# Kernel optimization log

Hardware: AMD Instinct MI355X
Metric: run time of the kernel (lower is better)

Reference implementation:

```python
import jax, jax.numpy as jnp
import numpy as np
import math

H, HD = 16, 64
EPS = 1e-6


def setup_inputs() -> dict:
    key = jax.random.key(0)
    ks = jax.random.split(key, 6)
    B, T, D = 4, 2048, 1024
    s = 0.02
    return {
        "x": jax.random.normal(ks[0], (B, T, D), jnp.float32),
        "wq": jax.random.normal(ks[1], (D, D), jnp.float32) * s,
        "wk": jax.random.normal(ks[2], (D, D), jnp.float32) * s,
        "wv": jax.random.normal(ks[3], (D, D), jnp.float32) * s,
        "wo": jax.random.normal(ks[4], (D, D), jnp.float32) * s,
        "norm_g": jnp.ones((D,), jnp.float32),
    }


def reference(x, wq, wk, wv, wo, norm_g):
    B, T, D = x.shape
    scale = math.sqrt(HD)
    # nn.Linear(D, D, bias=False): y = x @ W.T
    q = (x @ wq.T).reshape(B, T, H, HD).transpose(0, 2, 1, 3)  # [B,H,T,HD]
    k = (x @ wk.T).reshape(B, T, H, HD).transpose(0, 2, 1, 3)
    v = (x @ wv.T).reshape(B, T, H, HD).transpose(0, 2, 1, 3)
    scores = jnp.einsum("bhqd,bhkd->bhqk", q, k) / scale  # [B,H,T,T]
    causal = jnp.tril(jnp.ones((T, T), bool))  # True where allowed
    scores = jnp.where(causal, scores, -jnp.inf)
    attn = jax.nn.softmax(scores, axis=-1)  # dropout p=0 -> identity
    out = jnp.einsum("bhqk,bhkd->bhqd", attn, v)  # [B,H,T,HD]
    out = out.transpose(0, 2, 1, 3).reshape(B, T, D)
    y = x + out @ wo.T  # residual
    # RMSNorm
    rms = jnp.sqrt(jnp.mean(y * y, axis=-1, keepdims=True) + EPS)
    return (y / rms) * norm_g
```

## Files before the change

### kernel.cpp

```cpp
#include <hip/hip_runtime.h>
#include <hip/hip_bf16.h>

constexpr int NB  = 4;
constexpr int NT  = 2048;
constexpr int ND  = 1024;
constexpr int NH  = 16;
constexpr int NHD = 64;
constexpr int NM  = NB * NT;

typedef unsigned short u16;
typedef __attribute__((ext_vector_type(8))) short  short8;
typedef __attribute__((ext_vector_type(4))) float  f32x4;

__device__ __forceinline__ u16 f2bf(float f) {
  unsigned u = __builtin_bit_cast(unsigned, f);
  u += 0x7FFFu + ((u >> 16) & 1u);
  return (u16)(u >> 16);
}

__device__ __forceinline__ unsigned pk2bf(float lo, float hi_) {
  float2 t; t.x = lo; t.y = hi_;
  __hip_bfloat162 h2 = __float22bfloat162_rn(t);
  unsigned u;
  __builtin_memcpy(&u, &h2, 4);
  return u;
}

__device__ __forceinline__ void gll16(const u16* src, u16* dst) {
  __builtin_amdgcn_global_load_lds(
      (const __attribute__((address_space(1))) void*)src,
      (__attribute__((address_space(3))) void*)dst, 16, 0, 0);
}

__global__ __launch_bounds__(256) void cast_kernel(const float* __restrict__ in,
                                                   u16* __restrict__ out, int n4) {
  int i = blockIdx.x * 256 + threadIdx.x;
  if (i >= n4) return;
  float4 v = ((const float4*)in)[i];
  ushort4 o;
  o.x = f2bf(v.x); o.y = f2bf(v.y); o.z = f2bf(v.z); o.w = f2bf(v.w);
  ((ushort4*)out)[i] = o;
}

__global__ __launch_bounds__(256) void cast4_kernel(
    const float* __restrict__ w0, const float* __restrict__ w1,
    const float* __restrict__ w2, const float* __restrict__ w3,
    u16* __restrict__ o0, u16* __restrict__ o1,
    u16* __restrict__ o2, u16* __restrict__ o3) {
  const int z = blockIdx.x >> 10;
  const float* in = (z == 0) ? w0 : (z == 1) ? w1 : (z == 2) ? w2 : w3;
  u16* out       = (z == 0) ? o0 : (z == 1) ? o1 : (z == 2) ? o2 : o3;
  int i = (blockIdx.x & 1023) * 256 + threadIdx.x;
  float4 v = ((const float4*)in)[i];
  ushort4 o;
  o.x = f2bf(v.x); o.y = f2bf(v.y); o.z = f2bf(v.z); o.w = f2bf(v.w);
  ((ushort4*)out)[i] = o;
}

__global__ __launch_bounds__(512, 2) void gemm_qkv3(
    const u16* __restrict__ xb,
    const u16* __restrict__ wqb, const u16* __restrict__ wkb, const u16* __restrict__ wvb,
    u16* __restrict__ Qb, u16* __restrict__ Kb, u16* __restrict__ VTb) {
  const int z    = blockIdx.z;
  const int row0 = blockIdx.x << 7;
  const int col0 = blockIdx.y << 7;

  const u16* wsel = (z == 0) ? wqb : (z == 1) ? wkb : wvb;
  u16* osel      = (z == 0) ? Qb  : (z == 1) ? Kb  : VTb;
  const float scl = (z == 0) ? 0.125f * 1.44269504f : 1.0f;

  const int tid  = threadIdx.x;
  const int lane = tid & 63, wid = tid >> 6;
  const int wm = wid >> 2, wn = wid & 3;
  const int li = lane & 15, hi = lane >> 4;
  const int l3 = lane >> 3, sl = lane & 7;
  const int schunk = ((sl ^ l3) << 3);

  extern __shared__ __align__(16) u16 smem[];
  u16* lAb = smem;
  u16* lBb = smem + 3 * 128 * 64;

  auto stage = [&](int t) {
    const int bo = (t % 3) * 8192;
    const int k0 = t << 6;
#pragma unroll
    for (int h = 0; h < 2; ++h) {
      int r = h * 64 + wid * 8;
      gll16(&xb  [(size_t)(row0 + r + l3) * ND + k0 + schunk], &lAb[bo + r * 64]);
      gll16(&wsel[(size_t)(col0 + r + l3) * ND + k0 + schunk], &lBb[bo + r * 64]);
    }
  };

  f32x4 acc[4][2] = {};

  stage(0);
  stage(1);

  for (int i = 0; i < 16; ++i) {
    if (i < 15) { asm volatile("s_waitcnt vmcnt(4)" ::: "memory"); }
    else        { asm volatile("s_waitcnt vmcnt(0)" ::: "memory"); }
    __builtin_amdgcn_s_barrier();

    if (i + 2 < 16) stage(i + 2);

    const u16* la = &lAb[(i % 3) * 8192];
    const u16* lb = &lBb[(i % 3) * 8192];

    short8 a[4][2], b[2][2];
#pragma unroll
    for (int m = 0; m < 4; ++m)
#pragma unroll
      for (int c = 0; c < 2; ++c)
        a[m][c] = *(const short8*)&la[(wm * 64 + m * 16 + li) * 64 + (((c * 4 + hi) ^ (li & 7)) << 3)];
#pragma unroll
    for (int n = 0; n < 2; ++n)
#pragma unroll
      for (int c = 0; c < 2; ++c)
        b[n][c] = *(const short8*)&lb[(wn * 32 + n * 16 + li) * 64 + (((c * 4 + hi) ^ (li & 7)) << 3)];

    if (z == 2) {
#pragma unroll
      for (int m = 0; m < 4; ++m)
#pragma unroll
        for (int n = 0; n < 2; ++n)
#pragma unroll
          for (int c = 0; c < 2; ++c)
            acc[m][n] = __builtin_amdgcn_mfma_f32_16x16x32_bf16(a[m][c], b[n][c], acc[m][n], 0, 0, 0);
    } else {
#pragma unroll
      for (int m = 0; m < 4; ++m)
#pragma unroll
        for (int n = 0; n < 2; ++n)
#pragma unroll
          for (int c = 0; c < 2; ++c)
            acc[m][n] = __builtin_amdgcn_mfma_f32_16x16x32_bf16(b[n][c], a[m][c], acc[m][n], 0, 0, 0);
    }
  }

#pragma unroll
  for (int m = 0; m < 4; ++m)
#pragma unroll
    for (int n = 0; n < 2; ++n) {
      if (z == 2) {
        int token0 = row0 + wm * 64 + m * 16 + hi * 4;
        int col    = col0 + wn * 32 + n * 16 + li;
        int b_ = token0 >> 11, t0 = token0 & (NT - 1);
        int h_ = col >> 6,     d_ = col & (NHD - 1);
        uint2 w;
        w.x = pk2bf(acc[m][n][0], acc[m][n][1]);
        w.y = pk2bf(acc[m][n][2], acc[m][n][3]);
        *(uint2*)&osel[(((size_t)(b_ * NH + h_)) * NHD + d_) * NT + t0] = w;
      } else {
        int token = row0 + wm * 64 + m * 16 + li;
        int feat0 = col0 + wn * 32 + n * 16 + hi * 4;
        int b_ = token >> 11, t_ = token & (NT - 1);
        int h_ = feat0 >> 6,  d0 = feat0 & (NHD - 1);
        uint2 w;
        w.x = pk2bf(acc[m][n][0] * scl, acc[m][n][1] * scl);
        w.y = pk2bf(acc[m][n][2] * scl, acc[m][n][3] * scl);
        *(uint2*)&osel[(((size_t)(b_ * NH + h_)) * NT + t_) * NHD + d0] = w;
      }
    }
}

__global__ __launch_bounds__(512, 2) void gemm_wo3(
    const u16* __restrict__ ao, const u16* __restrict__ wob,
    const float* __restrict__ x, float* __restrict__ y) {
  const int row0 = blockIdx.x << 7;
  const int col0 = blockIdx.y << 7;

  const int tid  = threadIdx.x;
  const int lane = tid & 63, wid = tid >> 6;
  const int wm = wid >> 2, wn = wid & 3;
  const int li = lane & 15, hi = lane >> 4;
  const int l3 = lane >> 3, sl = lane & 7;
  const int schunk = ((sl ^ l3) << 3);

  extern __shared__ __align__(16) u16 smem[];
  u16* lAb = smem;
  u16* lBb = smem + 3 * 128 * 64;

  auto stage = [&](int t) {
    const int bo = (t % 3) * 8192;
    const int k0 = t << 6;
#pragma unroll
    for (int h = 0; h < 2; ++h) {
      int r = h * 64 + wid * 8;
      gll16(&ao [(size_t)(row0 + r + l3) * ND + k0 + schunk], &lAb[bo + r * 64]);
      gll16(&wob[(size_t)(col0 + r + l3) * ND + k0 + schunk], &lBb[bo + r * 64]);
    }
  };

  f32x4 acc[4][2] = {};

  stage(0);
  stage(1);

  for (int i = 0; i < 16; ++i) {
    if (i < 15) { asm volatile("s_waitcnt vmcnt(4)" ::: "memory"); }
    else        { asm volatile("s_waitcnt vmcnt(0)" ::: "memory"); }
    __builtin_amdgcn_s_barrier();

    if (i + 2 < 16) stage(i + 2);

    const u16* la = &lAb[(i % 3) * 8192];
    const u16* lb = &lBb[(i % 3) * 8192];

    short8 a[4][2], b[2][2];
#pragma unroll
    for (int m = 0; m < 4; ++m)
#pragma unroll
      for (int c = 0; c < 2; ++c)
        a[m][c] = *(const short8*)&la[(wm * 64 + m * 16 + li) * 64 + (((c * 4 + hi) ^ (li & 7)) << 3)];
#pragma unroll
    for (int n = 0; n < 2; ++n)
#pragma unroll
      for (int c = 0; c < 2; ++c)
        b[n][c] = *(const short8*)&lb[(wn * 32 + n * 16 + li) * 64 + (((c * 4 + hi) ^ (li & 7)) << 3)];

#pragma unroll
    for (int m = 0; m < 4; ++m)
#pragma unroll
      for (int n = 0; n < 2; ++n)
#pragma unroll
        for (int c = 0; c < 2; ++c)
          acc[m][n] = __builtin_amdgcn_mfma_f32_16x16x32_bf16(b[n][c], a[m][c], acc[m][n], 0, 0, 0);
  }

#pragma unroll
  for (int m = 0; m < 4; ++m)
#pragma unroll
    for (int n = 0; n < 2; ++n) {
      int token = row0 + wm * 64 + m * 16 + li;
      int feat0 = col0 + wn * 32 + n * 16 + hi * 4;
      size_t idx = (size_t)token * ND + feat0;
      float4 xv = *(const float4*)&x[idx];
      float4 o;
      o.x = acc[m][n][0] + xv.x; o.y = acc[m][n][1] + xv.y;
      o.z = acc[m][n][2] + xv.z; o.w = acc[m][n][3] + xv.w;
      *(float4*)&y[idx] = o;
    }
}

__global__ __launch_bounds__(256) void attn_kernel(
    const u16* __restrict__ Q, const u16* __restrict__ K, const u16* __restrict__ VT,
    u16* __restrict__ AO) {
  const int nb  = gridDim.x * gridDim.y;
  const int b0  = blockIdx.y * gridDim.x + blockIdx.x;
  const int L   = (b0 & 7) * (nb >> 3) + (b0 >> 3);
  const int qb  = 31 - (L & 31);
  const int bh  = L >> 5;

  const int tid = threadIdx.x;
  const int lane = tid & 63, wid = tid >> 6;
  const int li = lane & 15, hi = lane >> 4;
  const int r0 = qb * 64 + wid * 16;
  const int qrow = r0 + li;
  const size_t bK = (size_t)bh * NT * NHD;
  const size_t bV = (size_t)bh * NHD * NT;

  __shared__ __align__(16) u16 lK [2][64 * 64];
  __shared__ __align__(16) u16 lVT[2][64 * 64];
  __shared__ __align__(16) u16 lP [4][16 * 64];

  const int ch0 = tid, ch1 = tid + 256;
  const int d0 = (ch0 >> 3) * 64 + (((ch0 & 7) ^ ((ch0 >> 3) & 7)) << 3);
  const int d1 = (ch1 >> 3) * 64 + (((ch1 & 7) ^ ((ch1 >> 3) & 7)) << 3);
  const int vOff0 = (ch0 >> 3) * NT + (ch0 & 7) * 8;
  const int vOff1 = (ch1 >> 3) * NT + (ch1 & 7) * 8;

  uint4 gK0, gK1, gV0, gV1;
  auto issue = [&](int kt) {
    const u16* kp = K + bK + (size_t)kt * 4096;
    const u16* vp = VT + bV + kt * 64;
    gK0 = *(const uint4*)&kp[ch0 * 8];
    gK1 = *(const uint4*)&kp[ch1 * 8];
    gV0 = *(const uint4*)&vp[vOff0];
    gV1 = *(const uint4*)&vp[vOff1];
  };
  auto commit = [&](int buf) {
    *(uint4*)&lK [buf][d0] = gK0;
    *(uint4*)&lK [buf][d1] = gK1;
    *(uint4*)&lVT[buf][d0] = gV0;
    *(uint4*)&lVT[buf][d1] = gV1;
  };

  short8 qf[2];
#pragma unroll
  for (int c = 0; c < 2; ++c)
    qf[c] = *(const short8*)&Q[bK + (size_t)qrow * NHD + c * 32 + hi * 8];

  short8 vone;
#pragma unroll
  for (int e = 0; e < 8; ++e) vone[e] = (short)0x3F80;

  f32x4 o[4] = {};
  f32x4 o4 = {};

  issue(0);
  commit(0);
  __syncthreads();
  int buf = 0;

  const int pswz = (li & 7) << 1;

  for (int kt = 0; kt <= qb; ++kt) {
    if (kt < qb) issue(kt + 1);

    f32x4 s[4] = {};
    __builtin_amdgcn_s_setprio(1);
#pragma unroll
    for (int g = 0; g < 4; ++g)
#pragma unroll
      for (int c = 0; c < 2; ++c) {
        short8 kf = *(const short8*)&lK[buf][(g * 16 + li) * 64 + ((c * 4 + hi) ^ (li & 7)) * 8];
        s[g] = __builtin_amdgcn_mfma_f32_16x16x32_bf16(kf, qf[c], s[g], 0, 0, 0);
      }
    __builtin_amdgcn_s_setprio(0);

    if (kt == qb) {
#pragma unroll
      for (int g = 0; g < 4; ++g)
#pragma unroll
        for (int rg = 0; rg < 4; ++rg) {
          int kcol = kt * 64 + g * 16 + hi * 4 + rg;
          if (kcol > qrow) s[g][rg] = -INFINITY;
        }
    }

#pragma unroll
    for (int g = 0; g < 4; ++g) {
      float p0 = __builtin_amdgcn_exp2f(s[g][0]);
      float p1 = __builtin_amdgcn_exp2f(s[g][1]);
      float p2 = __builtin_amdgcn_exp2f(s[g][2]);
      float p3 = __builtin_amdgcn_exp2f(s[g][3]);
      uint2 w;
      w.x = pk2bf(p0, p1);
      w.y = pk2bf(p2, p3);
      int k8s = (g * 4 + hi) ^ pswz;
      *(uint2*)&lP[wid][li * 64 + k8s * 4] = w;
    }

    short8 pa[2];
#pragma unroll
    for (int c = 0; c < 2; ++c)
      pa[c] = *(const short8*)&lP[wid][li * 64 + ((c * 8 + hi * 2) ^ pswz) * 4];

    __builtin_amdgcn_s_setprio(1);
#pragma unroll
    for (int gd = 0; gd < 4; ++gd)
#pragma unroll
      for (int c = 0; c < 2; ++c) {
        short8 vf = *(const short8*)&lVT[buf][(gd * 16 + li) * 64 + ((c * 4 + hi) ^ (li & 7)) * 8];
        o[gd] = __builtin_amdgcn_mfma_f32_16x16x32_bf16(vf, pa[c], o[gd], 0, 0, 0);
      }
#pragma unroll
    for (int c = 0; c < 2; ++c)
      o4 = __builtin_amdgcn_mfma_f32_16x16x32_bf16(vone, pa[c], o4, 0, 0, 0);
    __builtin_amdgcn_s_setprio(0);

    if (kt < qb) commit(buf ^ 1);
    __syncthreads();
    buf ^= 1;
  }

  const int b_ = bh >> 4, h_ = bh & 15;
  const float inv = 1.0f / o4[0];
  const size_t rowbase = ((size_t)(b_ * NT + qrow)) * ND + h_ * 64;
#pragma unroll
  for (int gd = 0; gd < 4; ++gd) {
    uint2 w;
    w.x = pk2bf(o[gd][0] * inv, o[gd][1] * inv);
    w.y = pk2bf(o[gd][2] * inv, o[gd][3] * inv);
    *(uint2*)&AO[rowbase + gd * 16 + hi * 4] = w;
  }
}

__global__ __launch_bounds__(256) void rmsnorm_kernel(float* __restrict__ y,
                                                      const float* __restrict__ g) {
  const int row = blockIdx.x;
  const int tid = threadIdx.x;
  const int lane = tid & 63, wid = tid >> 6;
  float4 v = ((const float4*)(y + (size_t)row * ND))[tid];
  float ss = v.x * v.x + v.y * v.y + v.z * v.z + v.w * v.w;
#pragma unroll
  for (int off = 32; off; off >>= 1) ss += __shfl_down(ss, off);
  __shared__ float red[4];
  if (lane == 0) red[wid] = ss;
  __syncthreads();
  float tot = red[0] + red[1] + red[2] + red[3];
  float inv = rsqrtf(tot * (1.0f / (float)ND) + 1e-6f);
  float4 gg = ((const float4*)g)[tid];
  float4 o;
  o.x = v.x * inv * gg.x; o.y = v.y * inv * gg.y;
  o.z = v.z * inv * gg.z; o.w = v.w * inv * gg.w;
  ((float4*)(y + (size_t)row * ND))[tid] = o;
}

extern "C" void kernel_launch(void* const* d_in, const int* in_sizes, int n_in,
                              void* d_out, int out_size, void* d_ws, size_t ws_size,
                              hipStream_t stream) {
  const float* x  = (const float*)d_in[0];
  const float* wq = (const float*)d_in[1];
  const float* wk = (const float*)d_in[2];
  const float* wv = (const float*)d_in[3];
  const float* wo = (const float*)d_in[4];
  const float* ng = (const float*)d_in[5];
  float* out = (float*)d_out;

  char* ws = (char*)d_ws;
  u16* xb  = (u16*)(ws);
  u16* wqb = (u16*)(ws + (16u << 20));
  u16* wkb = (u16*)(ws + (18u << 20));
  u16* wvb = (u16*)(ws + (20u << 20));
  u16* wob = (u16*)(ws + (22u << 20));
  u16* Qb  = (u16*)(ws + (24u << 20));
  u16* Kb  = (u16*)(ws + (40u << 20));
  u16* VTb = (u16*)(ws + (56u << 20));
  u16* AO  = (u16*)(ws + (72u << 20));

  cast_kernel<<<NM * ND / 4 / 256, 256, 0, stream>>>(x, xb, NM * ND / 4);
  cast4_kernel<<<4 * 1024, 256, 0, stream>>>(wq, wk, wv, wo, wqb, wkb, wvb, wob);

  gemm_qkv3<<<dim3(64, 8, 3), 512, 98304, stream>>>(xb, wqb, wkb, wvb, Qb, Kb, VTb);
  attn_kernel<<<dim3(NT / 64, NB * NH), 256, 0, stream>>>(Qb, Kb, VTb, AO);
  gemm_wo3<<<dim3(64, 8), 512, 98304, stream>>>(AO, wob, x, out);
  rmsnorm_kernel<<<NM, 256, 0, stream>>>(out, ng);
}
```

Measured before the change: 202.2 us.

## Software-pipeline attention PV matmul one tile behind QK and merge cast kernels

The attention loop now runs the P·V MFMAs for the previous key tile right after the QK^T MFMAs of the current tile. This lets the matrix unit overlap with the exp/softmax work, and the V tile buffer goes from double to triple buffering to support it. A tail block after the loop handles the final tile's PV. Separately, the x cast and the four weight-cast kernels are merged into one launch to save a kernel launch. This costs extra LDS and register pressure (the P fragments are carried across iterations), which may reduce occupancy.

```diff
diff --git a/kernel.cpp b/kernel.cpp
--- a/kernel.cpp
+++ b/kernel.cpp
@@ -32,25 +32,25 @@
       (__attribute__((address_space(3))) void*)dst, 16, 0, 0);
 }
 
-__global__ __launch_bounds__(256) void cast_kernel(const float* __restrict__ in,
-                                                   u16* __restrict__ out, int n4) {
-  int i = blockIdx.x * 256 + threadIdx.x;
-  if (i >= n4) return;
-  float4 v = ((const float4*)in)[i];
-  ushort4 o;
-  o.x = f2bf(v.x); o.y = f2bf(v.y); o.z = f2bf(v.z); o.w = f2bf(v.w);
-  ((ushort4*)out)[i] = o;
-}
-
-__global__ __launch_bounds__(256) void cast4_kernel(
+__global__ __launch_bounds__(256) void cast_all(
+    const float* __restrict__ x,
     const float* __restrict__ w0, const float* __restrict__ w1,
     const float* __restrict__ w2, const float* __restrict__ w3,
+    u16* __restrict__ xb,
     u16* __restrict__ o0, u16* __restrict__ o1,
     u16* __restrict__ o2, u16* __restrict__ o3) {
-  const int z = blockIdx.x >> 10;
-  const float* in = (z == 0) ? w0 : (z == 1) ? w1 : (z == 2) ? w2 : w3;
-  u16* out       = (z == 0) ? o0 : (z == 1) ? o1 : (z == 2) ? o2 : o3;
-  int i = (blockIdx.x & 1023) * 256 + threadIdx.x;
+  const int bid = blockIdx.x;
+  const float* in;
+  u16* out;
+  int i;
+  if (bid < 8192) {
+    in = x; out = xb; i = bid * 256 + threadIdx.x;
+  } else {
+    const int z = (bid - 8192) >> 10;
+    in  = (z == 0) ? w0 : (z == 1) ? w1 : (z == 2) ? w2 : w3;
+    out = (z == 0) ? o0 : (z == 1) ? o1 : (z == 2) ? o2 : o3;
+    i = ((bid - 8192) & 1023) * 256 + threadIdx.x;
+  }
   float4 v = ((const float4*)in)[i];
   ushort4 o;
   o.x = f2bf(v.x); o.y = f2bf(v.y); o.z = f2bf(v.z); o.w = f2bf(v.w);
@@ -260,7 +260,7 @@
   const size_t bV = (size_t)bh * NHD * NT;
 
   __shared__ __align__(16) u16 lK [2][64 * 64];
-  __shared__ __align__(16) u16 lVT[2][64 * 64];
+  __shared__ __align__(16) u16 lVT[3][64 * 64];
   __shared__ __align__(16) u16 lP [4][16 * 64];
 
   const int ch0 = tid, ch1 = tid + 256;
@@ -278,11 +278,11 @@
     gV0 = *(const uint4*)&vp[vOff0];
     gV1 = *(const uint4*)&vp[vOff1];
   };
-  auto commit = [&](int buf) {
-    *(uint4*)&lK [buf][d0] = gK0;
-    *(uint4*)&lK [buf][d1] = gK1;
-    *(uint4*)&lVT[buf][d0] = gV0;
-    *(uint4*)&lVT[buf][d1] = gV1;
+  auto commit = [&](int kt) {
+    *(uint4*)&lK [kt & 1][d0] = gK0;
+    *(uint4*)&lK [kt & 1][d1] = gK1;
+    *(uint4*)&lVT[kt % 3][d0] = gV0;
+    *(uint4*)&lVT[kt % 3][d1] = gV1;
   };
 
   short8 qf[2];
@@ -296,11 +296,11 @@
 
   f32x4 o[4] = {};
   f32x4 o4 = {};
+  short8 pap0, pap1;
 
   issue(0);
   commit(0);
   __syncthreads();
-  int buf = 0;
 
   const int pswz = (li & 7) << 1;
 
@@ -313,9 +313,22 @@
     for (int g = 0; g < 4; ++g)
 #pragma unroll
       for (int c = 0; c < 2; ++c) {
-        short8 kf = *(const short8*)&lK[buf][(g * 16 + li) * 64 + ((c * 4 + hi) ^ (li & 7)) * 8];
+        short8 kf = *(const short8*)&lK[kt & 1][(g * 16 + li) * 64 + ((c * 4 + hi) ^ (li & 7)) * 8];
         s[g] = __builtin_amdgcn_mfma_f32_16x16x32_bf16(kf, qf[c], s[g], 0, 0, 0);
       }
+
+    if (kt > 0) {
+      const u16* lv = lVT[(kt - 1) % 3];
+#pragma unroll
+      for (int gd = 0; gd < 4; ++gd) {
+        short8 vf0 = *(const short8*)&lv[(gd * 16 + li) * 64 + ((0 * 4 + hi) ^ (li & 7)) * 8];
+        short8 vf1 = *(const short8*)&lv[(gd * 16 + li) * 64 + ((1 * 4 + hi) ^ (li & 7)) * 8];
+        o[gd] = __builtin_amdgcn_mfma_f32_16x16x32_bf16(vf0, pap0, o[gd], 0, 0, 0);
+        o[gd] = __builtin_amdgcn_mfma_f32_16x16x32_bf16(vf1, pap1, o[gd], 0, 0, 0);
+      }
+      o4 = __builtin_amdgcn_mfma_f32_16x16x32_bf16(vone, pap0, o4, 0, 0, 0);
+      o4 = __builtin_amdgcn_mfma_f32_16x16x32_bf16(vone, pap1, o4, 0, 0, 0);
+    }
     __builtin_amdgcn_s_setprio(0);
 
     if (kt == qb) {
@@ -341,27 +354,24 @@
       *(uint2*)&lP[wid][li * 64 + k8s * 4] = w;
     }
 
-    short8 pa[2];
-#pragma unroll
-    for (int c = 0; c < 2; ++c)
-      pa[c] = *(const short8*)&lP[wid][li * 64 + ((c * 8 + hi * 2) ^ pswz) * 4];
-
-    __builtin_amdgcn_s_setprio(1);
-#pragma unroll
-    for (int gd = 0; gd < 4; ++gd)
-#pragma unroll
-      for (int c = 0; c < 2; ++c) {
-        short8 vf = *(const short8*)&lVT[buf][(gd * 16 + li) * 64 + ((c * 4 + hi) ^ (li & 7)) * 8];
-        o[gd] = __builtin_amdgcn_mfma_f32_16x16x32_bf16(vf, pa[c], o[gd], 0, 0, 0);
-      }
-#pragma unroll
-    for (int c = 0; c < 2; ++c)
-      o4 = __builtin_amdgcn_mfma_f32_16x16x32_bf16(vone, pa[c], o4, 0, 0, 0);
-    __builtin_amdgcn_s_setprio(0);
-
-    if (kt < qb) commit(buf ^ 1);
+    pap0 = *(const short8*)&lP[wid][li * 64 + ((0 * 8 + hi * 2) ^ pswz) * 4];
+    pap1 = *(const short8*)&lP[wid][li * 64 + ((1 * 8 + hi * 2) ^ pswz) * 4];
+
+    if (kt < qb) commit(kt + 1);
     __syncthreads();
-    buf ^= 1;
+  }
+
+  {
+    const u16* lv = lVT[qb % 3];
+#pragma unroll
+    for (int gd = 0; gd < 4; ++gd) {
+      short8 vf0 = *(const short8*)&lv[(gd * 16 + li) * 64 + ((0 * 4 + hi) ^ (li & 7)) * 8];
+      short8 vf1 = *(const short8*)&lv[(gd * 16 + li) * 64 + ((1 * 4 + hi) ^ (li & 7)) * 8];
+      o[gd] = __builtin_amdgcn_mfma_f32_16x16x32_bf16(vf0, pap0, o[gd], 0, 0, 0);
+      o[gd] = __builtin_amdgcn_mfma_f32_16x16x32_bf16(vf1, pap1, o[gd], 0, 0, 0);
+    }
+    o4 = __builtin_amdgcn_mfma_f32_16x16x32_bf16(vone, pap0, o4, 0, 0, 0);
+    o4 = __builtin_amdgcn_mfma_f32_16x16x32_bf16(vone, pap1, o4, 0, 0, 0);
   }
 
   const int b_ = bh >> 4, h_ = bh & 15;
@@ -419,8 +429,7 @@
   u16* VTb = (u16*)(ws + (56u << 20));
   u16* AO  = (u16*)(ws + (72u << 20));
 
-  cast_kernel<<<NM * ND / 4 / 256, 256, 0, stream>>>(x, xb, NM * ND / 4);
-  cast4_kernel<<<4 * 1024, 256, 0, stream>>>(wq, wk, wv, wo, wqb, wkb, wvb, wob);
+  cast_all<<<8192 + 4096, 256, 0, stream>>>(x, wq, wk, wv, wo, xb, wqb, wkb, wvb, wob);
 
   gemm_qkv3<<<dim3(64, 8, 3), 512, 98304, stream>>>(xb, wqb, wkb, wvb, Qb, Kb, VTb);
   attn_kernel<<<dim3(NT / 64, NB * NH), 256, 0, stream>>>(Qb, Kb, VTb, AO);
```

After: 200.3 us (median of 2 runs). No clear change (-0.9%).
